# Performance work log

Measured on AMD Instinct MI355X. Metric: run time of the kernel, lower is better.

## Reference

```python
import math
import jax, jax.numpy as jnp
import numpy as np

B_SZ, N_TOK, D_INNER, S_STATE = 4, 1024, 384, 16
DT_MAX = 0.15


def setup_inputs() -> dict:
    key = jax.random.key(0)
    ks = jax.random.split(key, 10)
    dt_init = math.log(math.exp(0.1) - 1.0)  # softplus^-1(0.1)
    x = jax.random.normal(ks[0], (B_SZ, N_TOK, D_INNER), dtype=jnp.float32)
    dt_self_W = jax.random.uniform(ks[1], (D_INNER, D_INNER), minval=-1e-4, maxval=1e-4)
    dt_self_b = jnp.full((D_INNER,), dt_init, dtype=jnp.float32)
    dt_diff_W = jax.random.uniform(ks[2], (D_INNER, D_INNER), minval=-1e-4, maxval=1e-4)
    dt_diff_b = jnp.full((D_INNER,), dt_init, dtype=jnp.float32)
    B_W = jax.random.normal(ks[3], (D_INNER, S_STATE)) / math.sqrt(D_INNER)
    C_real_W = jax.random.normal(ks[4], (D_INNER, S_STATE)) / math.sqrt(D_INNER)
    C_imag_W = jax.random.normal(ks[5], (D_INNER, S_STATE)) / math.sqrt(D_INNER)
    D_param = jnp.ones((D_INNER,), dtype=jnp.float32)
    A_log = jnp.broadcast_to(jnp.log(jnp.arange(1, S_STATE + 1, dtype=jnp.float32))[None, :], (D_INNER, S_STATE))
    lap = jnp.array([[0.0, 1.0, 0.0], [1.0, -4.0, 1.0], [0.0, 1.0, 0.0]], dtype=jnp.float32) * 0.1
    conv_w = jnp.broadcast_to(lap[None, None], (D_INNER, 1, 3, 3)) + 0.01 * jax.random.normal(ks[6], (D_INNER, 1, 3, 3))
    reaction_alpha = 0.01 * jax.random.normal(ks[7], (1, 1, D_INNER, 1))
    reaction_beta = 0.01 * jax.random.normal(ks[8], (1, 1, D_INNER, 1))
    return {
        'x': x, 'dt_self_W': dt_self_W, 'dt_self_b': dt_self_b,
        'dt_diff_W': dt_diff_W, 'dt_diff_b': dt_diff_b,
        'B_W': B_W, 'C_real_W': C_real_W, 'C_imag_W': C_imag_W,
        'D_param': D_param, 'A_log': A_log, 'conv_w': conv_w,
        'reaction_alpha': reaction_alpha, 'reaction_beta': reaction_beta,
        'K_steps': 2,
    }


def _laplacian(h, conv_w, H, W):
    # h: (B, N, D, S) -> depthwise 3x3 conv with replicate pad over the HxW grid
    B, N, D, S = h.shape
    hs = h.transpose(0, 3, 2, 1).reshape(B * S, D, H, W)
    hp = jnp.pad(hs, ((0, 0), (0, 0), (1, 1), (1, 1)), mode='edge')
    lap = jax.lax.conv_general_dilated(
        hp, conv_w, window_strides=(1, 1), padding='VALID',
        feature_group_count=D, dimension_numbers=('NCHW', 'OIHW', 'NCHW'))
    return lap.reshape(B, S, D, N).transpose(0, 3, 2, 1)


def reference(x, dt_self_W, dt_self_b, dt_diff_W, dt_diff_b, B_W, C_real_W,
              C_imag_W, D_param, A_log, conv_w, reaction_alpha, reaction_beta,
              K_steps):
    B, N, D = x.shape
    H = Wg = int(math.sqrt(N))
    A = -jax.nn.softplus(A_log)  # (D, S)
    delta_s = jnp.minimum(jax.nn.softplus(x @ dt_self_W.T + dt_self_b), DT_MAX)[..., None]
    delta_d = jnp.minimum(jax.nn.softplus(x @ dt_diff_W.T + dt_diff_b), DT_MAX)[..., None]
    B_mat = x @ B_W          # (B, N, S)
    C_real = x @ C_real_W    # (B, N, S)
    C_imag = x @ C_imag_W    # (B, N, S)
    mamba_input = jnp.einsum('bnd,bns->bnds', x, B_mat)
    h_real = mamba_input
    h_imag = jnp.zeros_like(h_real)
    dt = 1.0 / K_steps
    A_exp = A[None, None]  # (1,1,D,S)
    for _ in range(K_steps):
        f1_real = delta_s * (A_exp * h_real + mamba_input)
        f1_imag = delta_s * (A_exp * h_imag)
        lap_real = _laplacian(h_real, conv_w, H, Wg)
        lap_imag = _laplacian(h_imag, conv_w, H, Wg)
        f2_real = delta_d * -lap_imag
        f2_imag = delta_d * lap_real
        reaction_scale = reaction_alpha - reaction_beta * (h_real ** 2 + h_imag ** 2)
        h_real = h_real + dt * (f1_real + f2_real + h_real * reaction_scale)
        h_imag = h_imag + dt * (f1_imag + f2_imag + h_imag * reaction_scale)
    y = (jnp.einsum('bnds,bns->bnd', h_real, C_real)
         + jnp.einsum('bnds,bns->bnd', h_imag, C_imag)
         + x * D_param)
    return y
```

## Files before the change

kernel.cpp:

```cpp
#include <hip/hip_runtime.h>
#include <hip/hip_fp16.h>
#include <math.h>

#define B_SZ    4
#define N_TOKC  1024
#define D_INNER 384
#define S_STATE 16
#define DT_MAX_V 0.15f
#define PLANE   (B_SZ * N_TOKC)
#define DN      ((size_t)B_SZ * D_INNER * N_TOKC)

typedef __attribute__((ext_vector_type(8))) short bf16x8;
typedef __attribute__((ext_vector_type(4))) float f32x4;

__device__ __forceinline__ float softplusf(float z) {
    return fmaxf(z, 0.f) + log1pf(expf(-fabsf(z)));
}

__device__ __forceinline__ unsigned short f2bf(float f) {
    unsigned u = __float_as_uint(f);
    unsigned r = (u + 0x7FFFu + ((u >> 16) & 1u)) >> 16;
    return (unsigned short)r;
}

__device__ __forceinline__ unsigned packh2(float a, float b) {
    __half2 h = __floats2half2_rn(a, b);
    union { __half2 h; unsigned u; } c; c.h = h; return c.u;
}
__device__ __forceinline__ __half2 uph2(unsigned u) {
    union { unsigned u; __half2 h; } c; c.u = u; return c.h;
}

__device__ __forceinline__ size_t frag_off(int T, int kb, int q, int l16) {
    return ((size_t)((T * 12 + kb) * 4 + q)) * 128 + l16 * 8;
}

__device__ __forceinline__ bf16x8 pack8(const float* v) {
    bf16x8 o;
#pragma unroll
    for (int e = 0; e < 8; e++) o[e] = (short)f2bf(v[e]);
    return o;
}

__global__ __launch_bounds__(256) void k_prep(
    const float* __restrict__ x, const float* __restrict__ Ws, const float* __restrict__ Wd,
    const float* __restrict__ BW, const float* __restrict__ CrW, const float* __restrict__ CiW,
    const float* __restrict__ A_log,
    float* __restrict__ x_t, unsigned short* __restrict__ xp,
    unsigned short* __restrict__ Wdtp, unsigned short* __restrict__ Wbcp,
    float* __restrict__ A_tab)
{
    const int t = threadIdx.x;
    const int bx = blockIdx.x;
    if (bx < 1536) {
        __shared__ __align__(16) float tile[32][36];
        const int tok0 = (bx & 127) * 32;
        const int d0   = (bx >> 7) * 32;
        const int b = tok0 >> 10, n0 = tok0 & 1023;
        {
            const int r = t >> 3, c4 = (t & 7) * 4;
            const float4 v = *(const float4*)(x + (size_t)(tok0 + r) * D_INNER + d0 + c4);
            tile[r][c4 + 0] = v.x; tile[r][c4 + 1] = v.y;
            tile[r][c4 + 2] = v.z; tile[r][c4 + 3] = v.w;
        }
        __syncthreads();
        {
            const int dr = t >> 3, n4 = (t & 7) * 4;
            float4 o;
            o.x = tile[n4 + 0][dr]; o.y = tile[n4 + 1][dr];
            o.z = tile[n4 + 2][dr]; o.w = tile[n4 + 3][dr];
            *(float4*)(x_t + ((size_t)(b * D_INNER + d0 + dr)) * N_TOKC + n0 + n4) = o;
        }
        if (t < 128) {
            const int tt = t >> 6, q = (t >> 4) & 3, l16 = t & 15;
            const int row = tt * 16 + l16;
            float v[8];
#pragma unroll
            for (int e = 0; e < 8; e++) v[e] = tile[row][q * 8 + e];
            *(bf16x8*)(xp + frag_off((tok0 >> 4) + tt, d0 >> 5, q, l16)) = pack8(v);
        }
    } else if (bx < 1584) {
        const int vv = bx - 1536;
        const int mat = vv >= 24;
        const int dt16 = mat ? vv - 24 : vv;
        const float* W = mat ? Wd : Ws;
        unsigned short* dst = Wdtp + (size_t)mat * 147456;
#pragma unroll
        for (int it = 0; it < 3; it++) {
            const int item = t + it * 256;
            const int l16 = item & 15, q = (item >> 4) & 3, kb = item >> 6;
            const float* src = W + (size_t)(dt16 * 16 + l16) * D_INNER + kb * 32 + q * 8;
            float v[8];
            const float4 v0 = *(const float4*)(src);
            const float4 v1 = *(const float4*)(src + 4);
            v[0] = v0.x; v[1] = v0.y; v[2] = v0.z; v[3] = v0.w;
            v[4] = v1.x; v[5] = v1.y; v[6] = v1.z; v[7] = v1.w;
            *(bf16x8*)(dst + frag_off(dt16, kb, q, l16)) = pack8(v);
        }
    } else if (bx < 1587) {
        const int m = bx - 1584;
        const float* W2 = (m == 0) ? BW : ((m == 1) ? CrW : CiW);
#pragma unroll
        for (int it = 0; it < 3; it++) {
            const int item = t + it * 256;
            const int l16 = item & 15, q = (item >> 4) & 3, kb = item >> 6;
            float v[8];
#pragma unroll
            for (int e = 0; e < 8; e++)
                v[e] = W2[(size_t)(kb * 32 + q * 8 + e) * S_STATE + l16];
            *(bf16x8*)(Wbcp + (size_t)m * 6144 + frag_off(0, kb, q, l16)) = pack8(v);
        }
    } else {
        for (int i = t; i < D_INNER * S_STATE; i += 256)
            A_tab[i] = -softplusf(A_log[i]);
    }
}

__global__ __launch_bounds__(256) void k_gemm(
    const unsigned short* __restrict__ xp, const unsigned short* __restrict__ Wdtp,
    const unsigned short* __restrict__ Wbcp,
    const float* __restrict__ bs, const float* __restrict__ bd,
    unsigned* __restrict__ dsdd_t,
    float* __restrict__ Bm_t, unsigned* __restrict__ cri_t)
{
    const int wave = threadIdx.x >> 6;
    const int lane = threadIdx.x & 63;
    const int quad = lane >> 4, l16 = lane & 15;

    if (blockIdx.x < 384) {
        const int dbase = (blockIdx.x >> 6) * 64;
        const int tbase = (blockIdx.x & 63) * 64;
        const int wd = (wave & 1) * 32;
        const int wt = (wave >> 1) * 32;
        const int dT0 = (dbase + wd) >> 4;
        const int tT0 = (tbase + wt) >> 4;

        f32x4 acc[2][2][2];
#pragma unroll
        for (int m = 0; m < 2; m++)
#pragma unroll
            for (int i = 0; i < 2; i++)
#pragma unroll
                for (int j = 0; j < 2; j++) acc[m][i][j] = (f32x4)0.f;

        bf16x8 a0[2][2], b0[2];
#pragma unroll
        for (int m = 0; m < 2; m++)
#pragma unroll
            for (int i = 0; i < 2; i++)
                a0[m][i] = *(const bf16x8*)(Wdtp + (size_t)m * 147456
                                            + frag_off(dT0 + i, 0, quad, l16));
#pragma unroll
        for (int j = 0; j < 2; j++)
            b0[j] = *(const bf16x8*)(xp + frag_off(tT0 + j, 0, quad, l16));

#pragma unroll 2
        for (int kb = 0; kb < 12; kb++) {
            bf16x8 a1[2][2], b1[2];
            const int kn = (kb < 11) ? kb + 1 : 11;
#pragma unroll
            for (int m = 0; m < 2; m++)
#pragma unroll
                for (int i = 0; i < 2; i++)
                    a1[m][i] = *(const bf16x8*)(Wdtp + (size_t)m * 147456
                                                + frag_off(dT0 + i, kn, quad, l16));
#pragma unroll
            for (int j = 0; j < 2; j++)
                b1[j] = *(const bf16x8*)(xp + frag_off(tT0 + j, kn, quad, l16));

#pragma unroll
            for (int m = 0; m < 2; m++)
#pragma unroll
                for (int i = 0; i < 2; i++)
#pragma unroll
                    for (int j = 0; j < 2; j++)
                        acc[m][i][j] = __builtin_amdgcn_mfma_f32_16x16x32_bf16(
                            a0[m][i], b0[j], acc[m][i][j], 0, 0, 0);

#pragma unroll
            for (int m = 0; m < 2; m++)
#pragma unroll
                for (int i = 0; i < 2; i++) a0[m][i] = a1[m][i];
#pragma unroll
            for (int j = 0; j < 2; j++) b0[j] = b1[j];
        }

#pragma unroll
        for (int i = 0; i < 2; i++)
#pragma unroll
            for (int j = 0; j < 2; j++) {
                const int tok = tbase + wt + j * 16 + l16;
                const int bb = tok >> 10, n = tok & 1023;
#pragma unroll
                for (int reg = 0; reg < 4; reg++) {
                    const int d = dbase + wd + i * 16 + quad * 4 + reg;
                    const float vs = fminf(softplusf(acc[0][i][j][reg] + bs[d]), DT_MAX_V);
                    const float vd = fminf(softplusf(acc[1][i][j][reg] + bd[d]), DT_MAX_V);
                    dsdd_t[((size_t)(bb * D_INNER + d)) * N_TOKC + n] = packh2(vs, vd);
                }
            }
    } else {
        const int tT = (blockIdx.x - 384) * 4 + wave;
        f32x4 acc[3];
#pragma unroll
        for (int m = 0; m < 3; m++) acc[m] = (f32x4)0.f;

#pragma unroll 1
        for (int kb = 0; kb < 12; kb++) {
            const bf16x8 b = *(const bf16x8*)(xp + frag_off(tT, kb, quad, l16));
#pragma unroll
            for (int m = 0; m < 3; m++) {
                const bf16x8 a = *(const bf16x8*)(Wbcp + (size_t)m * 6144
                                                  + frag_off(0, kb, quad, l16));
                acc[m] = __builtin_amdgcn_mfma_f32_16x16x32_bf16(a, b, acc[m], 0, 0, 0);
            }
        }

        const int tok = tT * 16 + l16;
#pragma unroll
        for (int reg = 0; reg < 4; reg++) {
            const int s = quad * 4 + reg;
            Bm_t [(size_t)s * PLANE + tok] = acc[0][reg];
            cri_t[(size_t)s * PLANE + tok] = packh2(acc[1][reg], acc[2][reg]);
        }
    }
}

#define PSTRIDE 33
#define PSIZE   (PSTRIDE * 32)

__global__ __launch_bounds__(256) void k_ssm(
    const float* __restrict__ x_t, const float* __restrict__ conv_w, const float* __restrict__ A_tab,
    const float* __restrict__ ralpha, const float* __restrict__ rbeta, const float* __restrict__ Dp,
    const unsigned* __restrict__ dsdd_t,
    const float* __restrict__ Bm_t, const unsigned* __restrict__ cri_t,
    float* __restrict__ y_part)
{
    const int d  = blockIdx.x;
    const int b  = blockIdx.y;
    const int t  = threadIdx.x;
    const int c  = t & 31;
    const int g  = t >> 5;
    const int r0 = g * 4;

    __shared__ unsigned pl[4 * PSIZE];

    __half2 wh[9];
#pragma unroll
    for (int i = 0; i < 9; i++) wh[i] = __float2half2_rn(conv_w[d * 9 + i]);
    const float alpha = ralpha[d];
    const float beta  = rbeta[d];
    const float Dv    = Dp[d];

    const size_t base_dn = ((size_t)(b * D_INNER + d)) * N_TOKC;
    const size_t base_sn = (size_t)b * N_TOKC;

    float xv[4], dsv[4], ddv[4];
#pragma unroll
    for (int k = 0; k < 4; k++) {
        const int n = (r0 + k) * 32 + c;
        xv[k] = x_t[base_dn + n];
        const __half2 dd = uph2(dsdd_t[base_dn + n]);
        dsv[k] = __low2float(dd);
        ddv[k] = __high2float(dd);
    }

    int tapw[6][3];
    {
        const int cm = (c > 0)  ? c - 1 : 0;
        const int cp = (c < 31) ? c + 1 : 31;
        const int rtop = (r0 > 0)  ? r0 - 1 : 0;
        const int rbot = (r0 < 28) ? r0 + 4 : 31;
        int rowb[6];
        rowb[0] = rtop * PSTRIDE;
#pragma unroll
        for (int k = 0; k < 4; k++) rowb[k + 1] = (r0 + k) * PSTRIDE;
        rowb[5] = rbot * PSTRIDE;
#pragma unroll
        for (int rr = 0; rr < 6; rr++) {
            tapw[rr][0] = rowb[rr] + cm;
            tapw[rr][1] = rowb[rr] + c;
            tapw[rr][2] = rowb[rr] + cp;
        }
    }
    const int ws0 = r0 * PSTRIDE + c;

    float yp[4] = { 0.f, 0.f, 0.f, 0.f };

    for (int sg = 0; sg < 4; sg++) {
        float A[4];
#pragma unroll
        for (int s = 0; s < 4; s++) A[s] = A_tab[d * S_STATE + sg * 4 + s];

        float u[4][4], hr[4][4], hi[4][4];
#pragma unroll
        for (int k = 0; k < 4; k++) {
            const int n = (r0 + k) * 32 + c;
#pragma unroll
            for (int s = 0; s < 4; s++) {
                u[k][s]  = xv[k] * Bm_t[(size_t)(sg * 4 + s) * PLANE + base_sn + n];
                hr[k][s] = u[k][s];
            }
        }

#pragma unroll
        for (int p = 0; p < 2; p++)
#pragma unroll
            for (int k = 0; k < 4; k++)
                pl[p * PSIZE + ws0 + k * PSTRIDE] = packh2(hr[k][2 * p], hr[k][2 * p + 1]);
        __syncthreads();

#pragma unroll
        for (int p = 0; p < 2; p++) {
            __half2 tp[6][3];
#pragma unroll
            for (int rr = 0; rr < 6; rr++)
#pragma unroll
                for (int j = 0; j < 3; j++)
                    tp[rr][j] = uph2(pl[p * PSIZE + tapw[rr][j]]);
#pragma unroll
            for (int k = 0; k < 4; k++) {
                __half2 ac = __float2half2_rn(0.f);
#pragma unroll
                for (int a = 0; a < 3; a++)
#pragma unroll
                    for (int j = 0; j < 3; j++)
                        ac = __hfma2(wh[a * 3 + j], tp[k + a][j], ac);
                const float lap[2] = { __low2float(ac), __high2float(ac) };
#pragma unroll
                for (int e = 0; e < 2; e++) {
                    const int s = 2 * p + e;
                    const float hrv = hr[k][s];
                    const float f1r = dsv[k] * fmaf(A[s], hrv, u[k][s]);
                    const float rs  = fmaf(-beta, hrv * hrv, alpha);
                    hr[k][s] = hrv + 0.5f * (f1r + hrv * rs);
                    hi[k][s] = 0.5f * ddv[k] * lap[e];
                }
            }
        }
        __syncthreads();

#pragma unroll
        for (int s = 0; s < 4; s++)
#pragma unroll
            for (int k = 0; k < 4; k++)
                pl[s * PSIZE + ws0 + k * PSTRIDE] = packh2(hr[k][s], hi[k][s]);
        __syncthreads();

#pragma unroll
        for (int s = 0; s < 4; s++) {
            __half2 cri[4];
#pragma unroll
            for (int k = 0; k < 4; k++)
                cri[k] = uph2(cri_t[(size_t)(sg * 4 + s) * PLANE + base_sn + (r0 + k) * 32 + c]);
            __half2 tp[6][3];
#pragma unroll
            for (int rr = 0; rr < 6; rr++)
#pragma unroll
                for (int j = 0; j < 3; j++)
                    tp[rr][j] = uph2(pl[s * PSIZE + tapw[rr][j]]);
#pragma unroll
            for (int k = 0; k < 4; k++) {
                __half2 ac = __float2half2_rn(0.f);
#pragma unroll
                for (int a = 0; a < 3; a++)
#pragma unroll
                    for (int j = 0; j < 3; j++)
                        ac = __hfma2(wh[a * 3 + j], tp[k + a][j], ac);
                const float lapr = __low2float(ac);
                const float lapi = __high2float(ac);
                const float hrv = hr[k][s], hiv = hi[k][s];
                const float f1r = dsv[k] * fmaf(A[s], hrv, u[k][s]);
                const float f1i = dsv[k] * (A[s] * hiv);
                const float f2r = -ddv[k] * lapi;
                const float f2i =  ddv[k] * lapr;
                const float q   = fmaf(hrv, hrv, hiv * hiv);
                const float rs  = fmaf(-beta, q, alpha);
                const float nhr = hrv + 0.5f * (f1r + f2r + hrv * rs);
                const float nhi = hiv + 0.5f * (f1i + f2i + hiv * rs);
                yp[k] = fmaf(nhr, __low2float(cri[k]), yp[k]);
                yp[k] = fmaf(nhi, __high2float(cri[k]), yp[k]);
            }
        }
        if (sg < 3) __syncthreads();
    }

#pragma unroll
    for (int k = 0; k < 4; k++)
        y_part[base_dn + (r0 + k) * 32 + c] = fmaf(xv[k], Dv, yp[k]);
}

__global__ __launch_bounds__(256) void k_reduce(
    const float* __restrict__ y_part, float* __restrict__ y)
{
    const int d0 = blockIdx.x * 32;
    const int n0 = blockIdx.y * 32;
    const int b  = blockIdx.z;
    const int t  = threadIdx.x;
    __shared__ __align__(16) float tile[32][36];

    const int dr = t >> 3, nc4 = (t & 7) * 4;
    const float4 v = *(const float4*)(y_part
        + ((size_t)(b * D_INNER + d0 + dr)) * N_TOKC + n0 + nc4);
    tile[dr][nc4 + 0] = v.x; tile[dr][nc4 + 1] = v.y;
    tile[dr][nc4 + 2] = v.z; tile[dr][nc4 + 3] = v.w;
    __syncthreads();

    const int nr = t >> 3, dc4 = (t & 7) * 4;
    float4 o;
    o.x = tile[dc4 + 0][nr];
    o.y = tile[dc4 + 1][nr];
    o.z = tile[dc4 + 2][nr];
    o.w = tile[dc4 + 3][nr];
    *(float4*)(y + ((size_t)(b * N_TOKC + n0 + nr)) * D_INNER + d0 + dc4) = o;
}

extern "C" void kernel_launch(void* const* d_in, const int* in_sizes, int n_in,
                              void* d_out, int out_size, void* d_ws, size_t ws_size,
                              hipStream_t stream)
{
    const float* x    = (const float*)d_in[0];
    const float* Ws   = (const float*)d_in[1];
    const float* bsb  = (const float*)d_in[2];
    const float* Wd   = (const float*)d_in[3];
    const float* bdb  = (const float*)d_in[4];
    const float* BW   = (const float*)d_in[5];
    const float* CrW  = (const float*)d_in[6];
    const float* CiW  = (const float*)d_in[7];
    const float* Dp   = (const float*)d_in[8];
    const float* Alog = (const float*)d_in[9];
    const float* cw   = (const float*)d_in[10];
    const float* ra   = (const float*)d_in[11];
    const float* rb   = (const float*)d_in[12];
    float* y = (float*)d_out;

    float* ws = (float*)d_ws;
    unsigned* dsdd_t = (unsigned*)ws;
    float* x_t    = ws + DN;
    float* Bm_t   = x_t + DN;
    unsigned* cri_t = (unsigned*)(Bm_t + (size_t)S_STATE * PLANE);
    float* A_tab  = (float*)(cri_t + (size_t)S_STATE * PLANE);
    float* y_part = A_tab + (size_t)D_INNER * S_STATE;

    unsigned short* xp   = (unsigned short*)(y_part + DN);
    unsigned short* Wdtp = xp + (size_t)256 * 12 * 4 * 128;
    unsigned short* Wbcp = Wdtp + (size_t)2 * 147456;

    k_prep<<<dim3(1588), 256, 0, stream>>>(x, Ws, Wd, BW, CrW, CiW, Alog,
                                           x_t, xp, Wdtp, Wbcp, A_tab);
    k_gemm<<<dim3(448), 256, 0, stream>>>(xp, Wdtp, Wbcp, bsb, bdb,
                                          dsdd_t, Bm_t, cri_t);
    k_ssm<<<dim3(D_INNER, B_SZ), 256, 0, stream>>>(x_t, cw, A_tab, ra, rb, Dp,
                                                   dsdd_t, Bm_t, cri_t, y_part);
    k_reduce<<<dim3(12, 32, 4), 256, 0, stream>>>(y_part, y);
}
```

Measured before the change: 166.7 us.

## Fuse transpose-reduce into SSM kernel and tune occupancy with launch bounds

Removes the separate k_reduce transpose kernel and the y_part workspace, so the SSM kernel writes its output directly in (B,N,D) layout. This drops one launch and a full round trip of a B*D*N float buffer through memory. The trade-off is that each block writes with a stride of D_INNER floats, so its stores are uncoalesced scattered 4-byte writes. It also adds launch_bounds min-blocks 6 and disables unrolling of the state-group loop, to limit register pressure and raise occupancy, at some risk of spills.

```diff
diff --git a/kernel.cpp b/kernel.cpp
--- a/kernel.cpp
+++ b/kernel.cpp
@@ -229,12 +229,12 @@
 #define PSTRIDE 33
 #define PSIZE   (PSTRIDE * 32)
 
-__global__ __launch_bounds__(256) void k_ssm(
+__global__ __launch_bounds__(256, 6) void k_ssm(
     const float* __restrict__ x_t, const float* __restrict__ conv_w, const float* __restrict__ A_tab,
     const float* __restrict__ ralpha, const float* __restrict__ rbeta, const float* __restrict__ Dp,
     const unsigned* __restrict__ dsdd_t,
     const float* __restrict__ Bm_t, const unsigned* __restrict__ cri_t,
-    float* __restrict__ y_part)
+    float* __restrict__ y)
 {
     const int d  = blockIdx.x;
     const int b  = blockIdx.y;
@@ -287,6 +287,7 @@
 
     float yp[4] = { 0.f, 0.f, 0.f, 0.f };
 
+#pragma unroll 1
     for (int sg = 0; sg < 4; sg++) {
         float A[4];
 #pragma unroll
@@ -386,33 +387,10 @@
     }
 
 #pragma unroll
-    for (int k = 0; k < 4; k++)
-        y_part[base_dn + (r0 + k) * 32 + c] = fmaf(xv[k], Dv, yp[k]);
-}
-
-__global__ __launch_bounds__(256) void k_reduce(
-    const float* __restrict__ y_part, float* __restrict__ y)
-{
-    const int d0 = blockIdx.x * 32;
-    const int n0 = blockIdx.y * 32;
-    const int b  = blockIdx.z;
-    const int t  = threadIdx.x;
-    __shared__ __align__(16) float tile[32][36];
-
-    const int dr = t >> 3, nc4 = (t & 7) * 4;
-    const float4 v = *(const float4*)(y_part
-        + ((size_t)(b * D_INNER + d0 + dr)) * N_TOKC + n0 + nc4);
-    tile[dr][nc4 + 0] = v.x; tile[dr][nc4 + 1] = v.y;
-    tile[dr][nc4 + 2] = v.z; tile[dr][nc4 + 3] = v.w;
-    __syncthreads();
-
-    const int nr = t >> 3, dc4 = (t & 7) * 4;
-    float4 o;
-    o.x = tile[dc4 + 0][nr];
-    o.y = tile[dc4 + 1][nr];
-    o.z = tile[dc4 + 2][nr];
-    o.w = tile[dc4 + 3][nr];
-    *(float4*)(y + ((size_t)(b * N_TOKC + n0 + nr)) * D_INNER + d0 + dc4) = o;
+    for (int k = 0; k < 4; k++) {
+        const int n = (r0 + k) * 32 + c;
+        y[((size_t)(b * N_TOKC + n)) * D_INNER + d] = fmaf(xv[k], Dv, yp[k]);
+    }
 }
 
 extern "C" void kernel_launch(void* const* d_in, const int* in_sizes, int n_in,
@@ -440,9 +418,8 @@
     float* Bm_t   = x_t + DN;
     unsigned* cri_t = (unsigned*)(Bm_t + (size_t)S_STATE * PLANE);
     float* A_tab  = (float*)(cri_t + (size_t)S_STATE * PLANE);
-    float* y_part = A_tab + (size_t)D_INNER * S_STATE;
-
-    unsigned short* xp   = (unsigned short*)(y_part + DN);
+
+    unsigned short* xp   = (unsigned short*)(A_tab + (size_t)D_INNER * S_STATE);
     unsigned short* Wdtp = xp + (size_t)256 * 12 * 4 * 128;
     unsigned short* Wbcp = Wdtp + (size_t)2 * 147456;
 
@@ -451,6 +428,5 @@
     k_gemm<<<dim3(448), 256, 0, stream>>>(xp, Wdtp, Wbcp, bsb, bdb,
                                           dsdd_t, Bm_t, cri_t);
     k_ssm<<<dim3(D_INNER, B_SZ), 256, 0, stream>>>(x_t, cw, A_tab, ra, rb, Dp,
-                                                   dsdd_t, Bm_t, cri_t, y_part);
-    k_reduce<<<dim3(12, 32, 4), 256, 0, stream>>>(y_part, y);
-}
+                                                   dsdd_t, Bm_t, cri_t, y);
+}
```

After: 496.4 us. 198% more time.

## Use separate LDS planes per stage to drop barriers and spill state registers

Applied to the files above, without the earlier changes.

Expands shared memory from 4 to 6 planes so the step-1 results are written directly into planes 2-5 while planes 0-1 hold the initial state. This removes one barrier per state group, and the end-of-loop barrier also goes, since the next iteration writes different planes. The u/hr/hi register arrays are replaced by recomputing u from x and Bm and reading h from the fp16 LDS center tap. Together with unroll 1, this lowers register pressure. In exchange, the second step now uses fp16-rounded h values (a precision change) and LDS per block grows by half, which may reduce occupancy.

```diff
diff --git a/kernel.cpp b/kernel.cpp
--- a/kernel.cpp
+++ b/kernel.cpp
@@ -243,7 +243,7 @@
     const int g  = t >> 5;
     const int r0 = g * 4;
 
-    __shared__ unsigned pl[4 * PSIZE];
+    __shared__ unsigned pl[6 * PSIZE];
 
     __half2 wh[9];
 #pragma unroll
@@ -287,27 +287,27 @@
 
     float yp[4] = { 0.f, 0.f, 0.f, 0.f };
 
+#pragma unroll 1
     for (int sg = 0; sg < 4; sg++) {
         float A[4];
 #pragma unroll
         for (int s = 0; s < 4; s++) A[s] = A_tab[d * S_STATE + sg * 4 + s];
 
-        float u[4][4], hr[4][4], hi[4][4];
+        float Bmf[4][4];
 #pragma unroll
         for (int k = 0; k < 4; k++) {
             const int n = (r0 + k) * 32 + c;
 #pragma unroll
-            for (int s = 0; s < 4; s++) {
-                u[k][s]  = xv[k] * Bm_t[(size_t)(sg * 4 + s) * PLANE + base_sn + n];
-                hr[k][s] = u[k][s];
-            }
+            for (int s = 0; s < 4; s++)
+                Bmf[k][s] = Bm_t[(size_t)(sg * 4 + s) * PLANE + base_sn + n];
         }
 
 #pragma unroll
         for (int p = 0; p < 2; p++)
 #pragma unroll
             for (int k = 0; k < 4; k++)
-                pl[p * PSIZE + ws0 + k * PSTRIDE] = packh2(hr[k][2 * p], hr[k][2 * p + 1]);
+                pl[p * PSIZE + ws0 + k * PSTRIDE]
+                    = packh2(xv[k] * Bmf[k][2 * p], xv[k] * Bmf[k][2 * p + 1]);
         __syncthreads();
 
 #pragma unroll
@@ -330,21 +330,15 @@
 #pragma unroll
                 for (int e = 0; e < 2; e++) {
                     const int s = 2 * p + e;
-                    const float hrv = hr[k][s];
-                    const float f1r = dsv[k] * fmaf(A[s], hrv, u[k][s]);
-                    const float rs  = fmaf(-beta, hrv * hrv, alpha);
-                    hr[k][s] = hrv + 0.5f * (f1r + hrv * rs);
-                    hi[k][s] = 0.5f * ddv[k] * lap[e];
+                    const float u   = xv[k] * Bmf[k][s];
+                    const float f1r = dsv[k] * fmaf(A[s], u, u);
+                    const float rs  = fmaf(-beta, u * u, alpha);
+                    const float nhr = u + 0.5f * (f1r + u * rs);
+                    const float nhi = 0.5f * ddv[k] * lap[e];
+                    pl[(2 + s) * PSIZE + ws0 + k * PSTRIDE] = packh2(nhr, nhi);
                 }
             }
         }
-        __syncthreads();
-
-#pragma unroll
-        for (int s = 0; s < 4; s++)
-#pragma unroll
-            for (int k = 0; k < 4; k++)
-                pl[s * PSIZE + ws0 + k * PSTRIDE] = packh2(hr[k][s], hi[k][s]);
         __syncthreads();
 
 #pragma unroll
@@ -358,7 +352,7 @@
             for (int rr = 0; rr < 6; rr++)
 #pragma unroll
                 for (int j = 0; j < 3; j++)
-                    tp[rr][j] = uph2(pl[s * PSIZE + tapw[rr][j]]);
+                    tp[rr][j] = uph2(pl[(2 + s) * PSIZE + tapw[rr][j]]);
 #pragma unroll
             for (int k = 0; k < 4; k++) {
                 __half2 ac = __float2half2_rn(0.f);
@@ -369,8 +363,10 @@
                         ac = __hfma2(wh[a * 3 + j], tp[k + a][j], ac);
                 const float lapr = __low2float(ac);
                 const float lapi = __high2float(ac);
-                const float hrv = hr[k][s], hiv = hi[k][s];
-                const float f1r = dsv[k] * fmaf(A[s], hrv, u[k][s]);
+                const float hrv = __low2float(tp[k + 1][1]);
+                const float hiv = __high2float(tp[k + 1][1]);
+                const float u   = xv[k] * Bmf[k][s];
+                const float f1r = dsv[k] * fmaf(A[s], hrv, u);
                 const float f1i = dsv[k] * (A[s] * hiv);
                 const float f2r = -ddv[k] * lapi;
                 const float f2i =  ddv[k] * lapr;
@@ -382,7 +378,6 @@
                 yp[k] = fmaf(nhi, __high2float(cri[k]), yp[k]);
             }
         }
-        if (sg < 3) __syncthreads();
     }
 
 #pragma unroll
```

New measurement: 161.9 us. 2.9% less time.
